# Performance work log

Measured on AMD Instinct MI355X. Metric: run time of the kernel, lower is better.

## Reference

```python
import jax, jax.numpy as jnp
import numpy as np

B_, T_, D_ = 4, 4096, 512
H_, DH_ = 8, 64
N_HASHES, BUCKET = 4, 64
SELF_ATTN_VAL = -5e4  # TOKEN_SELF_ATTN_VALUE from reformer-pytorch


def setup_inputs() -> dict:
    key = jax.random.key(0)
    ks = jax.random.split(key, 12)
    s = 0.02
    return {
        "src": jax.random.normal(ks[0], (B_, T_, D_), jnp.float32),
        "Wqk": jax.random.normal(ks[1], (D_, D_), jnp.float32) * s,
        "Wv": jax.random.normal(ks[2], (D_, D_), jnp.float32) * s,
        "Wout": jax.random.normal(ks[3], (D_, D_), jnp.float32) * s,
        "bout": jnp.zeros((D_,), jnp.float32),
        "W1": jax.random.normal(ks[4], (D_, 2048), jnp.float32) * s,
        "b1": jnp.zeros((2048,), jnp.float32),
        "W2": jax.random.normal(ks[5], (2048, D_), jnp.float32) * s,
        "b2": jnp.zeros((D_,), jnp.float32),
        "gamma": jnp.ones((D_,), jnp.float32),
        "beta": jnp.zeros((D_,), jnp.float32),
        "rotations": jax.random.normal(ks[6], (DH_, N_HASHES, (T_ // BUCKET) // 2), jnp.float32),
    }


def _look_one_back(x):
    # concat each chunk with the previous chunk (wraparound), along the slot axis
    prev = jnp.concatenate([x[:, -1:], x[:, :-1]], axis=1)
    return jnp.concatenate([x, prev], axis=2)


def lsh_attention(qk, v, rotations):
    # qk, v: (B, T, d) with B = batch*heads; shared-QK LSH attention (non-causal,
    # attend_across_buckets=True, allow_duplicate_attention=True, no dropout)
    B, T, d = qk.shape
    n_buckets = T // BUCKET
    # --- hashing ---
    rv = jnp.einsum("btf,fhi->bhti", qk, rotations)          # (B, n_hashes, T, nb/2)
    rv = jnp.concatenate([rv, -rv], axis=-1)                  # (B, n_hashes, T, nb)
    buckets = jnp.argmax(rv, axis=-1)                         # (B, n_hashes, T)
    offsets = (jnp.arange(N_HASHES) * n_buckets)[None, :, None]
    buckets = (buckets + offsets).reshape(B, N_HASHES * T)
    # --- sort by (bucket, position) ---
    ticker = jnp.arange(N_HASHES * T)
    buckets_and_t = buckets * T + (ticker % T)[None, :]
    sticker = jnp.argsort(buckets_and_t, axis=-1)             # (B, n_hashes*T)
    undo_sort = jnp.argsort(sticker, axis=-1)
    st = sticker % T
    sqk = jnp.take_along_axis(qk, st[..., None], axis=1)      # (B, n_hashes*T, d)
    sv = jnp.take_along_axis(v, st[..., None], axis=1)
    # --- chunk ---
    chunks = N_HASHES * n_buckets
    bq_t = st.reshape(B, chunks, BUCKET)
    bqk = sqk.reshape(B, chunks, BUCKET, d)
    bv = sv.reshape(B, chunks, BUCKET, d)
    bq = bqk
    bk = bqk / (jnp.linalg.norm(bqk, axis=-1, keepdims=True) + 1e-6)
    bk = _look_one_back(bk)                                   # (B, chunks, 2*BUCKET, d)
    bv = _look_one_back(bv)
    bkv_t = _look_one_back(bq_t)                              # (B, chunks, 2*BUCKET)
    # --- attention within chunk (+ one look-back chunk) ---
    dots = jnp.einsum("bcie,bcje->bcij", bq, bk) * (d ** -0.5)
    self_mask = bq_t[:, :, :, None] == bkv_t[:, :, None, :]
    dots = jnp.where(self_mask, SELF_ATTN_VAL, dots)
    lse = jax.nn.logsumexp(dots, axis=-1, keepdims=True)
    p = jnp.exp(dots - lse)
    bo = jnp.einsum("bcij,bcje->bcie", p, bv)
    # --- unsort and combine hash rounds ---
    so = bo.reshape(B, N_HASHES * T, d)
    slog = lse.reshape(B, N_HASHES * T)
    o = jnp.take_along_axis(so, undo_sort[..., None], axis=1)
    logits = jnp.take_along_axis(slog, undo_sort, axis=1)
    o = o.reshape(B, N_HASHES, T, d)
    logits = logits.reshape(B, N_HASHES, T, 1)
    probs = jnp.exp(logits - jax.nn.logsumexp(logits, axis=1, keepdims=True))
    return jnp.sum(o * probs, axis=1)                         # (B, T, d)


def _layer(src, Wqk, Wv, Wout, bout, W1, b1, W2, b2, gamma, beta, rotations):
    b, t, dm = src.shape
    qk = src @ Wqk
    v = src @ Wv
    def split(x):
        return x.reshape(b, t, H_, DH_).transpose(0, 2, 1, 3).reshape(b * H_, t, DH_)
    o = lsh_attention(split(qk), split(v), rotations)
    o = o.reshape(b, H_, t, DH_).transpose(0, 2, 1, 3).reshape(b, t, dm)
    attn_out = o @ Wout + bout
    x = src + attn_out                # residual (dropout = identity in eval)
    ffn = jax.nn.relu(x @ W1 + b1) @ W2 + b2
    y = x + ffn
    mu = jnp.mean(y, axis=-1, keepdims=True)
    var = jnp.mean((y - mu) ** 2, axis=-1, keepdims=True)
    return (y - mu) / jnp.sqrt(var + 1e-6) * gamma + beta     # post-norm (norm2)


def reference(src, Wqk, Wv, Wout, bout, W1, b1, W2, b2, gamma, beta, rotations):
    return _layer(src, Wqk, Wv, Wout, bout, W1, b1, W2, b2, gamma, beta, rotations)
```

## Files before the change

### kernel.cpp

```cpp
#include <hip/hip_runtime.h>

#define B_ 4
#define T_ 4096
#define D_ 512
#define H_ 8
#define DH_ 64
#define NH_ 4
#define NB_ 64
#define BH_ (B_*H_)
#define CHUNKS_ (NH_*NB_)
#define NTICK_ (NH_*T_)
#define M_ (B_*T_)
#define FFN_ 2048

typedef __attribute__((ext_vector_type(8))) short bf16x8;
typedef __attribute__((ext_vector_type(4))) float f32x4;

__device__ __forceinline__ unsigned short f2bf(float x) {
  unsigned int u = __float_as_uint(x);
  return (unsigned short)((u + 0x7FFFu + ((u >> 16) & 1u)) >> 16);
}
__device__ __forceinline__ float bf2f(unsigned short s) {
  return __uint_as_float(((unsigned int)s) << 16);
}
__device__ __forceinline__ unsigned int cvt_pk_bf16(float lo, float hi) {
  unsigned int r;
  asm("v_cvt_pk_bf16_f32 %0, %1, %2" : "=v"(r) : "v"(lo), "v"(hi));
  return r;
}

__device__ __forceinline__ void gld_lds16(const void* g, void* l) {
  __builtin_amdgcn_global_load_lds(
      (const __attribute__((address_space(1))) unsigned int*)g,
      (__attribute__((address_space(3))) unsigned int*)l, 16, 0, 0);
}

__device__ __forceinline__ int off64(int row, int k) {
  return row * 64 + (((k >> 3) ^ ((row ^ (row >> 3)) & 7)) << 3) + (k & 7);
}
__device__ __forceinline__ int off128(int row, int k) {
  return row * 128 + (((k >> 3) ^ ((row ^ (row >> 3)) & 7)) << 3) + (k & 7);
}

template<int BM, int OUT_MODE, bool HAS_BIAS, bool RELU, bool HAS_RESID, bool FUSE_INV>
__global__ __launch_bounds__(256) void gemm_bf16(
    const unsigned short* __restrict__ A, const unsigned short* __restrict__ BT,
    const float* __restrict__ bias, const unsigned short* __restrict__ resid,
    float* __restrict__ Cf, unsigned short* __restrict__ Cb,
    float* __restrict__ invn,
    int M, int N, int K, int lda, int ldbt, int ldr)
{
  constexpr int MI = BM / 32;
  __shared__ __align__(16) unsigned short smem[(BM + 128) * 64];
  unsigned short* As = smem;
  unsigned short* Bs = smem + BM * 64;
  const int tid = threadIdx.x;
  const int lane = tid & 63;
  const int w = tid >> 6;
  const int wm = (w >> 1) * (BM / 2), wn = (w & 1) * 64;
  const int g = lane >> 4, cl = lane & 15;

  const int gx = gridDim.x;
  const int id = blockIdx.x + blockIdx.y * gx;
  const int cpx = (gx * gridDim.y) >> 3;
  const int swz = (id & 7) * cpx + (id >> 3);
  const int m0 = (swz / gx) * BM, n0 = (swz % gx) * 128;

  f32x4 acc[MI][4];
#pragma unroll
  for (int i = 0; i < MI; ++i)
#pragma unroll
    for (int j = 0; j < 4; ++j) acc[i][j] = (f32x4){0.f, 0.f, 0.f, 0.f};

  const int srow = tid >> 3;
  const int skc  = (tid & 7) * 8;

  for (int k0 = 0; k0 < K; k0 += 64) {
#pragma unroll
    for (int ci = 0; ci < BM / 32; ++ci)
      gld_lds16(&A[(size_t)(m0 + ci * 32 + srow) * lda + k0 + skc],
                &As[ci * 2048 + tid * 8]);
#pragma unroll
    for (int ci = 0; ci < 4; ++ci)
      gld_lds16(&BT[(size_t)(n0 + ci * 32 + srow) * ldbt + k0 + skc],
                &Bs[ci * 2048 + tid * 8]);
    __syncthreads();
#pragma unroll
    for (int kk = 0; kk < 64; kk += 32) {
      bf16x8 af[MI], bfr[4];
#pragma unroll
      for (int i = 0; i < MI; ++i)
        af[i] = *(const bf16x8*)&As[(wm + i * 16 + cl) * 64 + kk + g * 8];
#pragma unroll
      for (int j = 0; j < 4; ++j)
        bfr[j] = *(const bf16x8*)&Bs[(wn + j * 16 + cl) * 64 + kk + g * 8];
#pragma unroll
      for (int i = 0; i < MI; ++i)
#pragma unroll
        for (int j = 0; j < 4; ++j)
          acc[i][j] = __builtin_amdgcn_mfma_f32_16x16x32_bf16(af[i], bfr[j], acc[i][j], 0, 0, 0);
    }
    __syncthreads();
  }

  float bv[4];
  if constexpr (HAS_BIAS) {
#pragma unroll
    for (int j = 0; j < 4; ++j) bv[j] = bias[n0 + wn + j * 16 + cl];
  }
#pragma unroll
  for (int i = 0; i < MI; ++i) {
#pragma unroll
    for (int r = 0; r < 4; ++r) {
      const int lrow = wm + i * 16 + g * 4 + r;
      float v4[4];
      float ss = 0.f;
#pragma unroll
      for (int j = 0; j < 4; ++j) {
        float val = acc[i][j][r];
        if constexpr (HAS_BIAS) val += bv[j];
        if constexpr (RELU) val = fmaxf(val, 0.f);
        v4[j] = val;
        if constexpr (FUSE_INV) ss += val * val;
        if constexpr (OUT_MODE == 2)
          Cf[(size_t)(m0 + lrow) * N + n0 + wn + j * 16 + cl] = val;
      }
      const unsigned int p01 = cvt_pk_bf16(v4[0], v4[1]);
      const unsigned int p23 = cvt_pk_bf16(v4[2], v4[3]);
      const int sw = (lrow & 7) << 3;
      smem[lrow * 128 + ((wn +  0 + cl) ^ sw)] = (unsigned short)p01;
      smem[lrow * 128 + ((wn + 16 + cl) ^ sw)] = (unsigned short)(p01 >> 16);
      smem[lrow * 128 + ((wn + 32 + cl) ^ sw)] = (unsigned short)p23;
      smem[lrow * 128 + ((wn + 48 + cl) ^ sw)] = (unsigned short)(p23 >> 16);
      if constexpr (FUSE_INV) {
        ss += __shfl_xor(ss, 1); ss += __shfl_xor(ss, 2);
        ss += __shfl_xor(ss, 4); ss += __shfl_xor(ss, 8);
        if (cl == 0) {
          const int m = m0 + lrow;
          const int bb = m >> 12, t = m & (T_ - 1);
          const int hh = ((n0 + wn) >> 6) & 7;
          invn[((size_t)(bb * 8 + hh)) * T_ + t] = 1.0f / (sqrtf(ss) + 1e-6f);
        }
      }
    }
  }
  __syncthreads();
#pragma unroll
  for (int l = 0; l < BM / 16; ++l) {
    const int idx = tid + l * 256;
    const int row = idx >> 4, c8 = (idx & 15) * 8;
    uint4 u = *(const uint4*)&smem[row * 128 + (c8 ^ ((row & 7) << 3))];
    if constexpr (HAS_RESID) {
      const uint4 rv = *(const uint4*)&resid[(size_t)(m0 + row) * ldr + n0 + c8];
      const unsigned short* sp = (const unsigned short*)&u;
      const unsigned short* rp = (const unsigned short*)&rv;
      float f[8];
#pragma unroll
      for (int e = 0; e < 8; ++e) f[e] = bf2f(sp[e]) + bf2f(rp[e]);
      u.x = cvt_pk_bf16(f[0], f[1]); u.y = cvt_pk_bf16(f[2], f[3]);
      u.z = cvt_pk_bf16(f[4], f[5]); u.w = cvt_pk_bf16(f[6], f[7]);
    }
    *(uint4*)&Cb[(size_t)(m0 + row) * N + n0 + c8] = u;
  }
}

__global__ __launch_bounds__(256) void prep_all(
    const float* __restrict__ Wqk, const float* __restrict__ Wv,
    const float* __restrict__ Wout, const float* __restrict__ W1,
    const float* __restrict__ W2, const float* __restrict__ src,
    unsigned short* __restrict__ WqkTp, unsigned short* __restrict__ WvT,
    unsigned short* __restrict__ WoutT, unsigned short* __restrict__ W1T,
    unsigned short* __restrict__ W2T, unsigned short* __restrict__ src_pair)
{
  __shared__ float tile[32][33];
  int bid = blockIdx.x;
  if (bid >= 2816) {
    const int i = (bid - 2816) * 256 + threadIdx.x;
    const int gpr = D_ >> 3;
    const int m = i / gpr, d0 = (i - m * gpr) * 8;
    float x[8];
    *(float4*)&x[0] = *(const float4*)&src[(size_t)m * D_ + d0];
    *(float4*)&x[4] = *(const float4*)&src[(size_t)m * D_ + d0 + 4];
    unsigned short hi[8], lo[8];
#pragma unroll
    for (int e = 0; e < 8; ++e) {
      hi[e] = f2bf(x[e]);
      lo[e] = f2bf(x[e] - bf2f(hi[e]));
    }
    *(uint4*)&src_pair[(size_t)m * 2 * D_ + d0]      = *(const uint4*)&hi[0];
    *(uint4*)&src_pair[(size_t)m * 2 * D_ + D_ + d0] = *(const uint4*)&lo[0];
    return;
  }
  const float* W; unsigned short* WT; int K, N, bx, by; bool split = false;
  if (bid < 256)        { W = Wqk;  WT = WqkTp; K = 512;  N = 512;  split = true;
                          bx = bid & 15; by = bid >> 4; }
  else if (bid < 512)   { bid -= 256;  W = Wv;   WT = WvT;   K = 512;  N = 512;
                          bx = bid & 15; by = bid >> 4; }
  else if (bid < 768)   { bid -= 512;  W = Wout; WT = WoutT; K = 512;  N = 512;
                          bx = bid & 15; by = bid >> 4; }
  else if (bid < 1792)  { bid -= 768;  W = W1;   WT = W1T;   K = 512;  N = 2048;
                          bx = bid & 63; by = bid >> 6; }
  else                  { bid -= 1792; W = W2;   WT = W2T;   K = 2048; N = 512;
                          bx = bid & 15; by = bid >> 4; }
  const int k0 = by * 32, n0 = bx * 32;
  const int tx = threadIdx.x & 31, ty = threadIdx.x >> 5;
#pragma unroll
  for (int r = 0; r < 32; r += 8)
    tile[ty + r][tx] = W[(size_t)(k0 + ty + r) * N + n0 + tx];
  __syncthreads();
  const int ld = split ? 2 * K : K;
#pragma unroll
  for (int r = 0; r < 32; r += 8) {
    const float x = tile[tx][ty + r];
    const unsigned short hi = f2bf(x);
    WT[(size_t)(n0 + ty + r) * ld + k0 + tx] = hi;
    if (split)
      WT[(size_t)(n0 + ty + r) * ld + K + k0 + tx] = f2bf(x - bf2f(hi));
  }
}

__global__ __launch_bounds__(256) void hash_gemm_kernel(
    const float* __restrict__ qk, const float* __restrict__ rot,
    int* __restrict__ buckets)
{
  __shared__ __align__(16) float As[64][136];
  __shared__ __align__(16) float Bs[64][132];
  const int tid = threadIdx.x;
  const int tx = tid & 15, ty = tid >> 4;
  const int t0 = blockIdx.x * 128, bh = blockIdx.y;
  const int b = bh >> 3, hd = bh & 7;

#pragma unroll
  for (int l = 0; l < 8; ++l) {
    const int idx = tid + l * 256;
    const int row = idx >> 4;
    const int kq = (idx & 15) << 2;
    const float4 a = *(const float4*)&qk[((size_t)b * T_ + t0 + row) * D_ + hd * DH_ + kq];
    As[kq + 0][row] = a.x; As[kq + 1][row] = a.y;
    As[kq + 2][row] = a.z; As[kq + 3][row] = a.w;
  }
#pragma unroll
  for (int l = 0; l < 8; ++l) {
    const int idx = tid + l * 256;
    const int kr = idx >> 5;
    const int c4 = (idx & 31) << 2;
    *(float4*)&Bs[kr][c4] = *(const float4*)&rot[kr * 128 + c4];
  }
  __syncthreads();

  float acc[8][8];
#pragma unroll
  for (int i = 0; i < 8; ++i)
#pragma unroll
    for (int j = 0; j < 8; ++j) acc[i][j] = 0.f;

#pragma unroll 4
  for (int kk = 0; kk < 64; ++kk) {
    float a[8], bq[8];
    *(float4*)&a[0]  = *(const float4*)&As[kk][ty * 8];
    *(float4*)&a[4]  = *(const float4*)&As[kk][ty * 8 + 4];
    *(float4*)&bq[0] = *(const float4*)&Bs[kk][tx * 8];
    *(float4*)&bq[4] = *(const float4*)&Bs[kk][tx * 8 + 4];
#pragma unroll
    for (int i = 0; i < 8; ++i)
#pragma unroll
      for (int j = 0; j < 8; ++j)
        acc[i][j] = fmaf(a[i], bq[j], acc[i][j]);
  }
  __syncthreads();

  float* pval = &As[0][0];
  int*   pidx = (int*)&Bs[0][0];
  const int i0 = (tx & 3) * 8;
#pragma unroll
  for (int r = 0; r < 8; ++r) {
    float v = -3.0e38f; int idx = 127;
#pragma unroll
    for (int j = 0; j < 8; ++j) {
      const float p = acc[r][j];
      const int li = i0 + j;
      if (p > v || (p == v && li < idx)) { v = p; idx = li; }
      const float n = -p;
      const int ni = 32 + li;
      if (n > v || (n == v && ni < idx)) { v = n; idx = ni; }
    }
    pval[(ty * 8 + r) * 16 + tx] = v;
    pidx[(ty * 8 + r) * 16 + tx] = idx;
  }
  __syncthreads();

#pragma unroll
  for (int l = 0; l < 2; ++l) {
    const int id = tid + l * 256;
    const int tok = id >> 2, hh = id & 3;
    float v = pval[tok * 16 + hh * 4];
    int idx = pidx[tok * 16 + hh * 4];
#pragma unroll
    for (int e = 1; e < 4; ++e) {
      const float ov = pval[tok * 16 + hh * 4 + e];
      const int oi = pidx[tok * 16 + hh * 4 + e];
      if (ov > v || (ov == v && oi < idx)) { v = ov; idx = oi; }
    }
    buckets[((size_t)bh * NH_ + hh) * T_ + t0 + tok] = idx + hh * NB_;
  }
}

__global__ __launch_bounds__(256) void hist_kernel(
    const int* __restrict__ buckets, int* __restrict__ bstart)
{
  __shared__ int bins[256];
  const int bh = blockIdx.x;
  bins[threadIdx.x] = 0;
  __syncthreads();
  for (int e = threadIdx.x; e < NTICK_; e += 256)
    atomicAdd(&bins[buckets[(size_t)bh * NTICK_ + e]], 1);
  __syncthreads();
  if (threadIdx.x == 0) {
    int run = 0;
    for (int i = 0; i < 256; ++i) { const int c = bins[i]; bins[i] = run; run += c; }
  }
  __syncthreads();
  bstart[bh * 256 + threadIdx.x] = bins[threadIdx.x];
}

__global__ __launch_bounds__(64) void compact_kernel(
    const int* __restrict__ buckets, const int* __restrict__ bstart,
    int* __restrict__ sticker)
{
  const int bucket = blockIdx.x, bh = blockIdx.y;
  const int h = bucket >> 6;
  const int lane = threadIdx.x;
  int base = bstart[bh * 256 + bucket];
  const int* bk = buckets + (size_t)bh * NTICK_ + (size_t)h * T_;
  for (int it = 0; it < 64; ++it) {
    const int t = it * 64 + lane;
    const bool m = (bk[t] == bucket);
    const unsigned long long bal = __ballot(m);
    if (m) {
      const int pos = base + __popcll(bal & ((1ull << lane) - 1ull));
      sticker[(size_t)bh * NTICK_ + pos] = h * T_ + t;
    }
    base += __popcll(bal);
  }
}

__global__ __launch_bounds__(256) void attn_kernel(
    const unsigned short* __restrict__ qkb, const unsigned short* __restrict__ vb,
    const int* __restrict__ sticker, const float* __restrict__ invn,
    unsigned short* __restrict__ orowsb, float* __restrict__ logits)
{
  __shared__ __align__(16) unsigned short Rs[128 * 64];
  __shared__ __align__(16) unsigned short Vs[128 * 64];
  __shared__ int tks[128];
  __shared__ float invs[128];

  const int cx = blockIdx.x;
  const int c = (cx & 7) * 32 + (cx >> 3);
  const int bh = blockIdx.y;
  const int b = bh >> 3, hd = bh & 7;
  const int tid = threadIdx.x;
  const int hr = c >> 6;
  const int w = tid >> 6, lane = tid & 63, g = lane >> 4, cl = lane & 15;

  if (tid < 128) {
    const int sc = (tid < 64) ? c : ((c + CHUNKS_ - 1) & (CHUNKS_ - 1));
    const int tick = sticker[(size_t)bh * NTICK_ + sc * 64 + (tid & 63)];
    const int t = tick & (T_ - 1);
    tks[tid] = t;
    invs[tid] = invn[bh * T_ + t];
  }
  __syncthreads();

#pragma unroll
  for (int l = 0; l < 4; ++l) {
    const int idx = tid + l * 256;
    const int row = idx >> 3, k0 = (idx & 7) * 8;
    const size_t gb = ((size_t)b * T_ + tks[row]) * D_ + hd * DH_ + k0;
    *(uint4*)&Rs[off64(row, k0)] = *(const uint4*)&qkb[gb];
    *(uint4*)&Vs[off64(row, k0)] = *(const uint4*)&vb[gb];
  }
  __syncthreads();

  f32x4 sacc[8];
#pragma unroll
  for (int j = 0; j < 8; ++j) sacc[j] = (f32x4){0.f, 0.f, 0.f, 0.f};
  __builtin_amdgcn_s_setprio(1);
#pragma unroll
  for (int kk = 0; kk < 2; ++kk) {
    const bf16x8 aq = *(const bf16x8*)&Rs[off64(w * 16 + cl, kk * 32 + g * 8)];
#pragma unroll
    for (int j = 0; j < 8; ++j) {
      const bf16x8 bk = *(const bf16x8*)&Rs[off64(j * 16 + cl, kk * 32 + g * 8)];
      sacc[j] = __builtin_amdgcn_mfma_f32_16x16x32_bf16(aq, bk, sacc[j], 0, 0, 0);
    }
  }
  __builtin_amdgcn_s_setprio(0);
  const int d0 = (tid & 15) * 4, tg = tid >> 4;
  unsigned int qw[8][2];
#pragma unroll
  for (int e = 0; e < 8; ++e) {
    const uint2 q = *(const uint2*)&Vs[off64(tg * 8 + e, d0)];
    qw[e][0] = q.x; qw[e][1] = q.y;
  }
  __syncthreads();

  {
    unsigned short col[4][8];
#pragma unroll
    for (int e = 0; e < 8; ++e) {
      col[0][e] = (unsigned short)(qw[e][0] & 0xffffu);
      col[1][e] = (unsigned short)(qw[e][0] >> 16);
      col[2][e] = (unsigned short)(qw[e][1] & 0xffffu);
      col[3][e] = (unsigned short)(qw[e][1] >> 16);
    }
#pragma unroll
    for (int dd = 0; dd < 4; ++dd)
      *(uint4*)&Vs[off128(d0 + dd, tg * 8)] = *(const uint4*)&col[dd][0];
  }

  float iv[8]; int tk[8];
#pragma unroll
  for (int j = 0; j < 8; ++j) {
    iv[j] = invs[j * 16 + cl] * 0.125f;
    tk[j] = tks[j * 16 + cl];
  }
  float pinv[4];
#pragma unroll
  for (int r = 0; r < 4; ++r) {
    const int row = w * 16 + g * 4 + r;
    const int tq = tks[row];
    float e8[8];
    float sum = 0.f;
#pragma unroll
    for (int j = 0; j < 8; ++j) {
      float e = __expf(sacc[j][r] * iv[j]);
      if (tq == tk[j]) e = 0.f;
      e8[j] = e;
      sum += e;
    }
    sum += __shfl_xor(sum, 1); sum += __shfl_xor(sum, 2);
    sum += __shfl_xor(sum, 4); sum += __shfl_xor(sum, 8);
    pinv[r] = 1.f / sum;
#pragma unroll
    for (int j = 0; j < 8; j += 2) {
      const unsigned int pk = cvt_pk_bf16(e8[j], e8[j + 1]);
      Rs[off128(row, j * 16 + cl)]       = (unsigned short)pk;
      Rs[off128(row, (j + 1) * 16 + cl)] = (unsigned short)(pk >> 16);
    }
    if (cl == 0)
      logits[((size_t)bh * T_ + tq) * NH_ + hr] = __logf(sum);
  }
  __syncthreads();

  f32x4 oacc[4];
#pragma unroll
  for (int jd = 0; jd < 4; ++jd) oacc[jd] = (f32x4){0.f, 0.f, 0.f, 0.f};
  __builtin_amdgcn_s_setprio(1);
#pragma unroll
  for (int ks = 0; ks < 4; ++ks) {
    const bf16x8 pa = *(const bf16x8*)&Rs[off128(w * 16 + cl, ks * 32 + g * 8)];
#pragma unroll
    for (int jd = 0; jd < 4; ++jd) {
      const bf16x8 vv = *(const bf16x8*)&Vs[off128(jd * 16 + cl, ks * 32 + g * 8)];
      oacc[jd] = __builtin_amdgcn_mfma_f32_16x16x32_bf16(pa, vv, oacc[jd], 0, 0, 0);
    }
  }
  __builtin_amdgcn_s_setprio(0);
  __syncthreads();

#pragma unroll
  for (int r = 0; r < 4; ++r) {
    const int row = w * 16 + g * 4 + r;
    const unsigned int q01 = cvt_pk_bf16(oacc[0][r] * pinv[r], oacc[1][r] * pinv[r]);
    const unsigned int q23 = cvt_pk_bf16(oacc[2][r] * pinv[r], oacc[3][r] * pinv[r]);
    Rs[off64(row,      cl)] = (unsigned short)q01;
    Rs[off64(row, 16 + cl)] = (unsigned short)(q01 >> 16);
    Rs[off64(row, 32 + cl)] = (unsigned short)q23;
    Rs[off64(row, 48 + cl)] = (unsigned short)(q23 >> 16);
  }
  __syncthreads();

#pragma unroll
  for (int l = 0; l < 2; ++l) {
    const int idx = tid + l * 256;
    const int row = idx >> 3, k0 = (idx & 7) * 8;
    *(uint4*)&orowsb[(((size_t)bh * T_ + tks[row]) * NH_ + hr) * DH_ + k0] =
        *(const uint4*)&Rs[off64(row, k0)];
  }
}

__global__ __launch_bounds__(256) void combine_kernel(
    const unsigned short* __restrict__ orowsb, const float* __restrict__ logits,
    unsigned short* __restrict__ ocombb)
{
  const int gid = blockIdx.x * 4 + (threadIdx.x >> 6);
  const int lane = threadIdx.x & 63;
  const int bh = gid >> 12, t = gid & (T_ - 1);
  const int b = bh >> 3, hd = bh & 7;
  const float4 lg = *(const float4*)&logits[((size_t)bh * T_ + t) * NH_];
  const float m = fmaxf(fmaxf(lg.x, lg.y), fmaxf(lg.z, lg.w));
  const float w0 = __expf(lg.x - m), w1 = __expf(lg.y - m);
  const float w2 = __expf(lg.z - m), w3 = __expf(lg.w - m);
  const float inv = 1.f / (w0 + w1 + w2 + w3);
  const size_t rb = ((size_t)bh * T_ + t) * (NH_ * DH_) + lane;
  const float o = w0 * bf2f(orowsb[rb])
                + w1 * bf2f(orowsb[rb + DH_])
                + w2 * bf2f(orowsb[rb + 2 * DH_])
                + w3 * bf2f(orowsb[rb + 3 * DH_]);
  ocombb[((size_t)b * T_ + t) * D_ + hd * DH_ + lane] = f2bf(o * inv);
}

__global__ __launch_bounds__(256) void ln_kernel(
    const unsigned short* __restrict__ yb, const float* __restrict__ gamma,
    const float* __restrict__ beta, float* __restrict__ out)
{
  const int row = blockIdx.x * 4 + (threadIdx.x >> 6);
  const int lane = threadIdx.x & 63;
  const size_t base = (size_t)row * D_ + lane * 8;
  const uint4 u = *(const uint4*)&yb[base];
  const unsigned short* up = (const unsigned short*)&u;
  float x[8];
#pragma unroll
  for (int i = 0; i < 8; ++i) x[i] = bf2f(up[i]);
  float s = 0.f;
#pragma unroll
  for (int i = 0; i < 8; ++i) s += x[i];
#pragma unroll
  for (int m = 32; m >= 1; m >>= 1) s += __shfl_xor(s, m);
  const float mu = s * (1.f / D_);
  float vs = 0.f;
#pragma unroll
  for (int i = 0; i < 8; ++i) { const float d = x[i] - mu; vs += d * d; }
#pragma unroll
  for (int m = 32; m >= 1; m >>= 1) vs += __shfl_xor(vs, m);
  const float rstd = rsqrtf(vs * (1.f / D_) + 1e-6f);
  float gm[8], bt[8];
  *(float4*)&gm[0] = *(const float4*)&gamma[lane * 8];
  *(float4*)&gm[4] = *(const float4*)&gamma[lane * 8 + 4];
  *(float4*)&bt[0] = *(const float4*)&beta[lane * 8];
  *(float4*)&bt[4] = *(const float4*)&beta[lane * 8 + 4];
  float o[8];
#pragma unroll
  for (int i = 0; i < 8; ++i) o[i] = (x[i] - mu) * rstd * gm[i] + bt[i];
  *(float4*)&out[base]     = make_float4(o[0], o[1], o[2], o[3]);
  *(float4*)&out[base + 4] = make_float4(o[4], o[5], o[6], o[7]);
}

extern "C" void kernel_launch(void* const* d_in, const int* in_sizes, int n_in,
                              void* d_out, int out_size, void* d_ws, size_t ws_size,
                              hipStream_t stream) {
  (void)in_sizes; (void)n_in; (void)out_size; (void)ws_size;
  const float* src   = (const float*)d_in[0];
  const float* Wqk   = (const float*)d_in[1];
  const float* Wv    = (const float*)d_in[2];
  const float* Wout  = (const float*)d_in[3];
  const float* bout  = (const float*)d_in[4];
  const float* W1    = (const float*)d_in[5];
  const float* b1    = (const float*)d_in[6];
  const float* W2    = (const float*)d_in[7];
  const float* b2    = (const float*)d_in[8];
  const float* gamma = (const float*)d_in[9];
  const float* beta  = (const float*)d_in[10];
  const float* rot   = (const float*)d_in[11];
  float* out = (float*)d_out;

  char* ws = (char*)d_ws;
  const size_t MB = 1024 * 1024;
  float*          qk       = (float*)(ws);
  unsigned short* src_pair = (unsigned short*)(ws + 32 * MB);
  unsigned short* v_b      = (unsigned short*)(ws + 64 * MB);
  unsigned short* orows_b  = (unsigned short*)(ws + 80 * MB);
  unsigned short* qk_b     = (unsigned short*)(ws + 144 * MB);
  char* p = ws + 160 * MB;
  float* logits  = (float*)p; p += (size_t)BH_ * NH_ * T_ * 4;
  int*   buckets = (int*)p;   p += (size_t)BH_ * NH_ * T_ * 4;
  int*   sticker = (int*)p;   p += (size_t)BH_ * NTICK_ * 4;
  int*   bstart  = (int*)p;   p += (size_t)BH_ * 256 * 4;
  float* invn    = (float*)p; p += (size_t)BH_ * T_ * 4;
  unsigned short* WvT    = (unsigned short*)p; p += (size_t)D_ * D_ * 2;
  unsigned short* WoutT  = (unsigned short*)p; p += (size_t)D_ * D_ * 2;
  unsigned short* W1T    = (unsigned short*)p; p += (size_t)FFN_ * D_ * 2;
  unsigned short* W2T    = (unsigned short*)p; p += (size_t)D_ * FFN_ * 2;
  unsigned short* WqkTp  = (unsigned short*)p; p += (size_t)D_ * 2 * D_ * 2;

  unsigned short* ocomb_b  = qk_b;
  unsigned short* x_b      = v_b;
  unsigned short* hidden_b = orows_b;
  unsigned short* ybuf_b   = (unsigned short*)ws;

  prep_all<<<2816 + M_ * D_ / 8 / 256, 256, 0, stream>>>(
      Wqk, Wv, Wout, W1, W2, src, WqkTp, WvT, WoutT, W1T, W2T, src_pair);

  gemm_bf16<64, 2, false, false, false, true><<<dim3(D_ / 128, M_ / 64), 256, 0, stream>>>(
      src_pair, WqkTp, nullptr, nullptr, qk, qk_b, invn, M_, D_, 2 * D_, 2 * D_, 2 * D_, 0);
  gemm_bf16<64, 1, false, false, false, false><<<dim3(D_ / 128, M_ / 64), 256, 0, stream>>>(
      src_pair, WvT, nullptr, nullptr, nullptr, v_b, nullptr, M_, D_, D_, 2 * D_, D_, 0);
  hash_gemm_kernel<<<dim3(T_ / 128, BH_), 256, 0, stream>>>(qk, rot, buckets);
  hist_kernel<<<BH_, 256, 0, stream>>>(buckets, bstart);
  compact_kernel<<<dim3(256, BH_), 64, 0, stream>>>(buckets, bstart, sticker);
  attn_kernel<<<dim3(CHUNKS_, BH_), 256, 0, stream>>>(
      qk_b, v_b, sticker, invn, orows_b, logits);
  combine_kernel<<<BH_ * T_ / 4, 256, 0, stream>>>(orows_b, logits, ocomb_b);
  gemm_bf16<64, 1, true, false, true, false><<<dim3(D_ / 128, M_ / 64), 256, 0, stream>>>(
      ocomb_b, WoutT, bout, src_pair, nullptr, x_b, nullptr, M_, D_, D_, D_, D_, 2 * D_);
  gemm_bf16<128, 1, true, true, false, false><<<dim3(FFN_ / 128, M_ / 128), 256, 0, stream>>>(
      x_b, W1T, b1, nullptr, nullptr, hidden_b, nullptr, M_, FFN_, D_, D_, D_, 0);
  gemm_bf16<64, 1, true, false, true, false><<<dim3(D_ / 128, M_ / 64), 256, 0, stream>>>(
      hidden_b, W2T, b2, x_b, nullptr, ybuf_b, nullptr, M_, D_, FFN_, FFN_, FFN_, D_);
  ln_kernel<<<M_ / 4, 256, 0, stream>>>(ybuf_b, gamma, beta, out);
}
```

Baseline: 369.8 us.

## Fuse QK/V GEMMs, fold hash-combine into Wout GEMM, async attention gathers

Merges the QK and V projections into one GEMM over a concatenated weight, with V tiles using half the K range so the lo-part pass is skipped. Removes the separate combine kernel by computing the softmax-weighted sum of the four hash outputs inside the Wout GEMM's A-tile load. The attention kernel's row gather now uses direct global-to-LDS loads with a swizzled source. Smaller GEMMs also move to 128-row tiles. The trade-off is more ALU work and synchronous loads in the Wout GEMM's load phase, and fewer blocks per GEMM.

Result: slower. 381.4 us (+3.1%).

```diff
diff --git a/kernel.cpp b/kernel.cpp
--- a/kernel.cpp
+++ b/kernel.cpp
@@ -35,18 +35,20 @@
       (__attribute__((address_space(3))) unsigned int*)l, 16, 0, 0);
 }
 
+__device__ __forceinline__ int swf(int row) { return (row ^ (row >> 3)) & 7; }
 __device__ __forceinline__ int off64(int row, int k) {
-  return row * 64 + (((k >> 3) ^ ((row ^ (row >> 3)) & 7)) << 3) + (k & 7);
+  return row * 64 + (((k >> 3) ^ swf(row)) << 3) + (k & 7);
 }
 __device__ __forceinline__ int off128(int row, int k) {
-  return row * 128 + (((k >> 3) ^ ((row ^ (row >> 3)) & 7)) << 3) + (k & 7);
-}
-
-template<int BM, int OUT_MODE, bool HAS_BIAS, bool RELU, bool HAS_RESID, bool FUSE_INV>
+  return row * 128 + (((k >> 3) ^ swf(row)) << 3) + (k & 7);
+}
+
+template<int BM, int MODE, bool HAS_BIAS, bool RELU, bool HAS_RESID, bool FUSE_COMB>
 __global__ __launch_bounds__(256) void gemm_bf16(
     const unsigned short* __restrict__ A, const unsigned short* __restrict__ BT,
     const float* __restrict__ bias, const unsigned short* __restrict__ resid,
     float* __restrict__ Cf, unsigned short* __restrict__ Cb,
+    unsigned short* __restrict__ Cb2, const float* __restrict__ lgin,
     float* __restrict__ invn,
     int M, int N, int K, int lda, int ldbt, int ldr)
 {
@@ -66,6 +68,9 @@
   const int swz = (id & 7) * cpx + (id >> 3);
   const int m0 = (swz / gx) * BM, n0 = (swz % gx) * 128;
 
+  const bool isv = (MODE == 3) && (n0 >= 512);
+  const int Keff = isv ? (K >> 1) : K;
+
   f32x4 acc[MI][4];
 #pragma unroll
   for (int i = 0; i < MI; ++i)
@@ -75,11 +80,46 @@
   const int srow = tid >> 3;
   const int skc  = (tid & 7) * 8;
 
-  for (int k0 = 0; k0 < K; k0 += 64) {
-#pragma unroll
-    for (int ci = 0; ci < BM / 32; ++ci)
-      gld_lds16(&A[(size_t)(m0 + ci * 32 + srow) * lda + k0 + skc],
-                &As[ci * 2048 + tid * 8]);
+  for (int k0 = 0; k0 < Keff; k0 += 64) {
+    if constexpr (FUSE_COMB) {
+      const int head = k0 >> 6;
+#pragma unroll
+      for (int ci = 0; ci < BM / 32; ++ci) {
+        const int m = m0 + ci * 32 + srow;
+        const int bb = m >> 12, t = m & (T_ - 1);
+        const size_t bht = (size_t)(bb * 8 + head) * T_ + t;
+        const float4 lg = *(const float4*)&lgin[bht * NH_];
+        const float mx = fmaxf(fmaxf(lg.x, lg.y), fmaxf(lg.z, lg.w));
+        const float w0 = __expf(lg.x - mx), w1 = __expf(lg.y - mx);
+        const float w2 = __expf(lg.z - mx), w3 = __expf(lg.w - mx);
+        const float wiv = 1.f / (w0 + w1 + w2 + w3);
+        const size_t ob = bht * (NH_ * DH_) + skc;
+        const uint4 u0 = *(const uint4*)&A[ob];
+        const uint4 u1 = *(const uint4*)&A[ob + DH_];
+        const uint4 u2 = *(const uint4*)&A[ob + 2 * DH_];
+        const uint4 u3 = *(const uint4*)&A[ob + 3 * DH_];
+        const unsigned short* p0 = (const unsigned short*)&u0;
+        const unsigned short* p1 = (const unsigned short*)&u1;
+        const unsigned short* p2 = (const unsigned short*)&u2;
+        const unsigned short* p3 = (const unsigned short*)&u3;
+        unsigned short op[8];
+#pragma unroll
+        for (int e = 0; e < 8; e += 2) {
+          const float a0 = (w0 * bf2f(p0[e]) + w1 * bf2f(p1[e])
+                          + w2 * bf2f(p2[e]) + w3 * bf2f(p3[e])) * wiv;
+          const float a1 = (w0 * bf2f(p0[e + 1]) + w1 * bf2f(p1[e + 1])
+                          + w2 * bf2f(p2[e + 1]) + w3 * bf2f(p3[e + 1])) * wiv;
+          const unsigned int pk = cvt_pk_bf16(a0, a1);
+          op[e] = (unsigned short)pk; op[e + 1] = (unsigned short)(pk >> 16);
+        }
+        *(uint4*)&As[ci * 2048 + tid * 8] = *(const uint4*)&op[0];
+      }
+    } else {
+#pragma unroll
+      for (int ci = 0; ci < BM / 32; ++ci)
+        gld_lds16(&A[(size_t)(m0 + ci * 32 + srow) * lda + k0 + skc],
+                  &As[ci * 2048 + tid * 8]);
+    }
 #pragma unroll
     for (int ci = 0; ci < 4; ++ci)
       gld_lds16(&BT[(size_t)(n0 + ci * 32 + srow) * ldbt + k0 + skc],
@@ -121,9 +161,12 @@
         if constexpr (HAS_BIAS) val += bv[j];
         if constexpr (RELU) val = fmaxf(val, 0.f);
         v4[j] = val;
-        if constexpr (FUSE_INV) ss += val * val;
-        if constexpr (OUT_MODE == 2)
-          Cf[(size_t)(m0 + lrow) * N + n0 + wn + j * 16 + cl] = val;
+        if constexpr (MODE == 3) {
+          if (!isv) {
+            ss += val * val;
+            Cf[(size_t)(m0 + lrow) * 512 + n0 + wn + j * 16 + cl] = val;
+          }
+        }
       }
       const unsigned int p01 = cvt_pk_bf16(v4[0], v4[1]);
       const unsigned int p23 = cvt_pk_bf16(v4[2], v4[3]);
@@ -132,14 +175,16 @@
       smem[lrow * 128 + ((wn + 16 + cl) ^ sw)] = (unsigned short)(p01 >> 16);
       smem[lrow * 128 + ((wn + 32 + cl) ^ sw)] = (unsigned short)p23;
       smem[lrow * 128 + ((wn + 48 + cl) ^ sw)] = (unsigned short)(p23 >> 16);
-      if constexpr (FUSE_INV) {
-        ss += __shfl_xor(ss, 1); ss += __shfl_xor(ss, 2);
-        ss += __shfl_xor(ss, 4); ss += __shfl_xor(ss, 8);
-        if (cl == 0) {
-          const int m = m0 + lrow;
-          const int bb = m >> 12, t = m & (T_ - 1);
-          const int hh = ((n0 + wn) >> 6) & 7;
-          invn[((size_t)(bb * 8 + hh)) * T_ + t] = 1.0f / (sqrtf(ss) + 1e-6f);
+      if constexpr (MODE == 3) {
+        if (!isv) {
+          ss += __shfl_xor(ss, 1); ss += __shfl_xor(ss, 2);
+          ss += __shfl_xor(ss, 4); ss += __shfl_xor(ss, 8);
+          if (cl == 0) {
+            const int m = m0 + lrow;
+            const int bb = m >> 12, t = m & (T_ - 1);
+            const int hh = ((n0 + wn) >> 6) & 7;
+            invn[((size_t)(bb * 8 + hh)) * T_ + t] = 1.0f / (sqrtf(ss) + 1e-6f);
+          }
         }
       }
     }
@@ -160,7 +205,14 @@
       u.x = cvt_pk_bf16(f[0], f[1]); u.y = cvt_pk_bf16(f[2], f[3]);
       u.z = cvt_pk_bf16(f[4], f[5]); u.w = cvt_pk_bf16(f[6], f[7]);
     }
-    *(uint4*)&Cb[(size_t)(m0 + row) * N + n0 + c8] = u;
+    if constexpr (MODE == 3) {
+      if (isv)
+        *(uint4*)&Cb2[(size_t)(m0 + row) * 512 + (n0 - 512) + c8] = u;
+      else
+        *(uint4*)&Cb[(size_t)(m0 + row) * 512 + n0 + c8] = u;
+    } else {
+      *(uint4*)&Cb[(size_t)(m0 + row) * N + n0 + c8] = u;
+    }
   }
 }
 
@@ -168,9 +220,9 @@
     const float* __restrict__ Wqk, const float* __restrict__ Wv,
     const float* __restrict__ Wout, const float* __restrict__ W1,
     const float* __restrict__ W2, const float* __restrict__ src,
-    unsigned short* __restrict__ WqkTp, unsigned short* __restrict__ WvT,
-    unsigned short* __restrict__ WoutT, unsigned short* __restrict__ W1T,
-    unsigned short* __restrict__ W2T, unsigned short* __restrict__ src_pair)
+    unsigned short* __restrict__ WqkvTp, unsigned short* __restrict__ WoutT,
+    unsigned short* __restrict__ W1T, unsigned short* __restrict__ W2T,
+    unsigned short* __restrict__ src_pair)
 {
   __shared__ float tile[32][33];
   int bid = blockIdx.x;
@@ -192,9 +244,10 @@
     return;
   }
   const float* W; unsigned short* WT; int K, N, bx, by; bool split = false;
-  if (bid < 256)        { W = Wqk;  WT = WqkTp; K = 512;  N = 512;  split = true;
+  if (bid < 256)        { W = Wqk;  WT = WqkvTp; K = 512;  N = 512;  split = true;
                           bx = bid & 15; by = bid >> 4; }
-  else if (bid < 512)   { bid -= 256;  W = Wv;   WT = WvT;   K = 512;  N = 512;
+  else if (bid < 512)   { bid -= 256;  W = Wv; WT = WqkvTp + (size_t)512 * 1024;
+                          K = 512; N = 512; split = true;
                           bx = bid & 15; by = bid >> 4; }
   else if (bid < 768)   { bid -= 512;  W = Wout; WT = WoutT; K = 512;  N = 512;
                           bx = bid & 15; by = bid >> 4; }
@@ -371,13 +424,17 @@
   }
   __syncthreads();
 
-#pragma unroll
-  for (int l = 0; l < 4; ++l) {
-    const int idx = tid + l * 256;
-    const int row = idx >> 3, k0 = (idx & 7) * 8;
-    const size_t gb = ((size_t)b * T_ + tks[row]) * D_ + hd * DH_ + k0;
-    *(uint4*)&Rs[off64(row, k0)] = *(const uint4*)&qkb[gb];
-    *(uint4*)&Vs[off64(row, k0)] = *(const uint4*)&vb[gb];
+  {
+    const int sr = lane >> 3, gq = lane & 7;
+#pragma unroll
+    for (int l = 0; l < 4; ++l) {
+      const int row = l * 32 + w * 8 + sr;
+      const size_t gb = ((size_t)b * T_ + tks[row]) * D_ + hd * DH_
+                      + ((gq ^ swf(row)) << 3);
+      const int dst = (l * 32 + w * 8) * 64 + lane * 8;
+      gld_lds16(&qkb[gb], &Rs[dst]);
+      gld_lds16(&vb[gb],  &Vs[dst]);
+    }
   }
   __syncthreads();
 
@@ -487,27 +544,6 @@
     *(uint4*)&orowsb[(((size_t)bh * T_ + tks[row]) * NH_ + hr) * DH_ + k0] =
         *(const uint4*)&Rs[off64(row, k0)];
   }
-}
-
-__global__ __launch_bounds__(256) void combine_kernel(
-    const unsigned short* __restrict__ orowsb, const float* __restrict__ logits,
-    unsigned short* __restrict__ ocombb)
-{
-  const int gid = blockIdx.x * 4 + (threadIdx.x >> 6);
-  const int lane = threadIdx.x & 63;
-  const int bh = gid >> 12, t = gid & (T_ - 1);
-  const int b = bh >> 3, hd = bh & 7;
-  const float4 lg = *(const float4*)&logits[((size_t)bh * T_ + t) * NH_];
-  const float m = fmaxf(fmaxf(lg.x, lg.y), fmaxf(lg.z, lg.w));
-  const float w0 = __expf(lg.x - m), w1 = __expf(lg.y - m);
-  const float w2 = __expf(lg.z - m), w3 = __expf(lg.w - m);
-  const float inv = 1.f / (w0 + w1 + w2 + w3);
-  const size_t rb = ((size_t)bh * T_ + t) * (NH_ * DH_) + lane;
-  const float o = w0 * bf2f(orowsb[rb])
-                + w1 * bf2f(orowsb[rb + DH_])
-                + w2 * bf2f(orowsb[rb + 2 * DH_])
-                + w3 * bf2f(orowsb[rb + 3 * DH_]);
-  ocombb[((size_t)b * T_ + t) * D_ + hd * DH_ + lane] = f2bf(o * inv);
 }
 
 __global__ __launch_bounds__(256) void ln_kernel(
@@ -572,40 +608,43 @@
   unsigned short* orows_b  = (unsigned short*)(ws + 80 * MB);
   unsigned short* qk_b     = (unsigned short*)(ws + 144 * MB);
   char* p = ws + 160 * MB;
-  float* logits  = (float*)p; p += (size_t)BH_ * NH_ * T_ * 4;
+  float* logits  = (float*)p; p += (size_t)BH_ * T_ * NH_ * 4;
   int*   buckets = (int*)p;   p += (size_t)BH_ * NH_ * T_ * 4;
   int*   sticker = (int*)p;   p += (size_t)BH_ * NTICK_ * 4;
   int*   bstart  = (int*)p;   p += (size_t)BH_ * 256 * 4;
   float* invn    = (float*)p; p += (size_t)BH_ * T_ * 4;
-  unsigned short* WvT    = (unsigned short*)p; p += (size_t)D_ * D_ * 2;
+  unsigned short* WqkvTp = (unsigned short*)p; p += (size_t)1024 * 1024 * 2;
   unsigned short* WoutT  = (unsigned short*)p; p += (size_t)D_ * D_ * 2;
   unsigned short* W1T    = (unsigned short*)p; p += (size_t)FFN_ * D_ * 2;
   unsigned short* W2T    = (unsigned short*)p; p += (size_t)D_ * FFN_ * 2;
-  unsigned short* WqkTp  = (unsigned short*)p; p += (size_t)D_ * 2 * D_ * 2;
-
-  unsigned short* ocomb_b  = qk_b;
+
   unsigned short* x_b      = v_b;
   unsigned short* hidden_b = orows_b;
   unsigned short* ybuf_b   = (unsigned short*)ws;
 
   prep_all<<<2816 + M_ * D_ / 8 / 256, 256, 0, stream>>>(
-      Wqk, Wv, Wout, W1, W2, src, WqkTp, WvT, WoutT, W1T, W2T, src_pair);
-
-  gemm_bf16<64, 2, false, false, false, true><<<dim3(D_ / 128, M_ / 64), 256, 0, stream>>>(
-      src_pair, WqkTp, nullptr, nullptr, qk, qk_b, invn, M_, D_, 2 * D_, 2 * D_, 2 * D_, 0);
-  gemm_bf16<64, 1, false, false, false, false><<<dim3(D_ / 128, M_ / 64), 256, 0, stream>>>(
-      src_pair, WvT, nullptr, nullptr, nullptr, v_b, nullptr, M_, D_, D_, 2 * D_, D_, 0);
+      Wqk, Wv, Wout, W1, W2, src, WqkvTp, WoutT, W1T, W2T, src_pair);
+
+  gemm_bf16<128, 3, false, false, false, false>
+      <<<dim3(1024 / 128, M_ / 128), 256, 0, stream>>>(
+      src_pair, WqkvTp, nullptr, nullptr, qk, qk_b, v_b, nullptr, invn,
+      M_, 1024, 2 * D_, 2 * D_, 2 * D_, 0);
   hash_gemm_kernel<<<dim3(T_ / 128, BH_), 256, 0, stream>>>(qk, rot, buckets);
   hist_kernel<<<BH_, 256, 0, stream>>>(buckets, bstart);
   compact_kernel<<<dim3(256, BH_), 64, 0, stream>>>(buckets, bstart, sticker);
   attn_kernel<<<dim3(CHUNKS_, BH_), 256, 0, stream>>>(
       qk_b, v_b, sticker, invn, orows_b, logits);
-  combine_kernel<<<BH_ * T_ / 4, 256, 0, stream>>>(orows_b, logits, ocomb_b);
-  gemm_bf16<64, 1, true, false, true, false><<<dim3(D_ / 128, M_ / 64), 256, 0, stream>>>(
-      ocomb_b, WoutT, bout, src_pair, nullptr, x_b, nullptr, M_, D_, D_, D_, D_, 2 * D_);
-  gemm_bf16<128, 1, true, true, false, false><<<dim3(FFN_ / 128, M_ / 128), 256, 0, stream>>>(
-      x_b, W1T, b1, nullptr, nullptr, hidden_b, nullptr, M_, FFN_, D_, D_, D_, 0);
-  gemm_bf16<64, 1, true, false, true, false><<<dim3(D_ / 128, M_ / 64), 256, 0, stream>>>(
-      hidden_b, W2T, b2, x_b, nullptr, ybuf_b, nullptr, M_, D_, FFN_, FFN_, FFN_, D_);
+  gemm_bf16<128, 1, true, false, true, true>
+      <<<dim3(D_ / 128, M_ / 128), 256, 0, stream>>>(
+      orows_b, WoutT, bout, src_pair, nullptr, x_b, nullptr, logits, nullptr,
+      M_, D_, D_, 0, D_, 2 * D_);
+  gemm_bf16<128, 1, true, true, false, false>
+      <<<dim3(FFN_ / 128, M_ / 128), 256, 0, stream>>>(
+      x_b, W1T, b1, nullptr, nullptr, hidden_b, nullptr, nullptr, nullptr,
+      M_, FFN_, D_, D_, D_, 0);
+  gemm_bf16<128, 1, true, false, true, false>
+      <<<dim3(D_ / 128, M_ / 128), 256, 0, stream>>>(
+      hidden_b, W2T, b2, x_b, nullptr, ybuf_b, nullptr, nullptr, nullptr,
+      M_, D_, FFN_, FFN_, FFN_, D_);
   ln_kernel<<<M_ / 4, 256, 0, stream>>>(ybuf_b, gamma, beta, out);
 }
```
